# Kernel optimization log

Measured on AMD Instinct MI355X. Metric: run time of the kernel, lower is better.

Reference implementation:

```python
import jax, jax.numpy as jnp
import numpy as np

S, B, C = 1024, 2, 20
COORD, NOOBJ, NPRED = 5.0, 0.5, 5


def setup_inputs() -> dict:
    key = jax.random.key(0)
    k1, k2, k3 = jax.random.split(key, 3)
    pred = jax.random.normal(k1, (S, S, B * NPRED + C), dtype=jnp.float32)
    # target: box part uniform in [0,1) (w,h must be >=0 for sqrt), classes one-hot
    box_t = jax.random.uniform(k2, (S, S, B * NPRED), dtype=jnp.float32)
    cls_idx = jax.random.randint(k3, (S, S), 0, C)
    cls_t = jax.nn.one_hot(cls_idx, C, dtype=jnp.float32)
    target = jnp.concatenate([box_t, cls_t], axis=-1)
    return {"pred": pred, "target": target}


def reference(pred, target):
    # boxes: [S, S, B, 5] with (conf, x, y, w, h)
    boxes_p = pred[..., : B * NPRED].reshape(S, S, B, NPRED)
    boxes_t = target[..., : B * NPRED].reshape(S, S, B, NPRED)

    conf_p, x_p, y_p = boxes_p[..., 0], boxes_p[..., 1], boxes_p[..., 2]
    w_p = jnp.sqrt(jnp.abs(boxes_p[..., 3]))
    h_p = jnp.sqrt(jnp.abs(boxes_p[..., 4]))

    conf_t, x_t, y_t = boxes_t[..., 0], boxes_t[..., 1], boxes_t[..., 2]
    w_t = jnp.sqrt(boxes_t[..., 3])
    h_t = jnp.sqrt(boxes_t[..., 4])

    xy_loss = jnp.sum((jnp.square(x_t - x_p) + jnp.square(y_t - y_p)) * conf_t)
    box_loss = jnp.sum((jnp.square(w_t - w_p) + jnp.square(h_t - h_p)) * conf_t)
    conf_sq = jnp.square(conf_t - conf_p)
    confidence_loss = jnp.sum(conf_sq * conf_t)
    noobj_confidence_loss = jnp.sum(conf_sq * (1.0 - conf_t))

    # class loss: only cells whose target class vector sums to exactly 1.0
    pred_cls = pred[..., B * NPRED :].reshape(S * S, C)
    tgt_cls = target[..., B * NPRED :].reshape(S * S, C)
    cell_mask = (jnp.sum(tgt_cls, axis=-1) == 1.0).astype(pred.dtype)  # [S*S]
    per_cell = jnp.sum(jnp.square(tgt_cls) - jnp.square(pred_cls), axis=-1)
    cls_loss = jnp.sum(per_cell * cell_mask)

    return COORD * xy_loss + COORD * box_loss + confidence_loss + noobj_confidence_loss + cls_loss
```

## Files before the change

kernel.cpp:

```cpp
#include <hip/hip_runtime.h>


constexpr int CH         = 30;
constexpr int NCELL      = 1024 * 1024;
constexpr int BLOCK      = 256;
constexpr int TILE_CELLS = 128;
constexpr int TPF        = TILE_CELLS * CH;
constexpr int GRID       = 512;
constexpr int NTILES     = NCELL / TILE_CELLS;
constexpr int NIT        = NTILES / GRID;

__device__ __forceinline__ float wave_reduce_sum(float v) {
#pragma unroll
    for (int off = 32; off > 0; off >>= 1)
        v += __shfl_down(v, off, 64);
    return v;
}

__global__ __launch_bounds__(BLOCK, 2) void yolo_partial_kernel(
        const float* __restrict__ pred,
        const float* __restrict__ tgt,
        float* __restrict__ partial) {
    __shared__ float4 sbuf4[2][2 * TPF / 4];

    const int tid  = threadIdx.x;
    const int wv   = tid >> 6;
    const int ln   = tid & 63;
    const int cell = tid >> 1;
    const int half = tid & 1;

    float4 p0, p1, p2, t0, t1, t2;
    float2 p3, t3;
    float  p4, t4;

#define LOAD_TILE(tile)                                                      \
    do {                                                                     \
        const size_t tb = (size_t)(tile) * TPF;                              \
        const float4* pf4 = reinterpret_cast<const float4*>(pred + tb);      \
        const float4* tf4 = reinterpret_cast<const float4*>(tgt  + tb);      \
        const float2* pf2 = reinterpret_cast<const float2*>(pred + tb);      \
        const float2* tf2 = reinterpret_cast<const float2*>(tgt  + tb);      \
        p0 = pf4[0 * 256 + tid];  t0 = tf4[0 * 256 + tid];                   \
        p1 = pf4[1 * 256 + tid];  t1 = tf4[1 * 256 + tid];                   \
        p2 = pf4[2 * 256 + tid];  t2 = tf4[2 * 256 + tid];                   \
        p3 = pf2[1536 + tid];     t3 = tf2[1536 + tid];                      \
        p4 = pred[tb + 3584 + tid]; t4 = tgt[tb + 3584 + tid];               \
    } while (0)

#define STORE_TILE(b)                                                        \
    do {                                                                     \
        float*  sf  = reinterpret_cast<float*>(&sbuf4[(b)][0]);              \
        float4* sp4 = reinterpret_cast<float4*>(sf);                         \
        float4* st4 = reinterpret_cast<float4*>(sf + TPF);                   \
        float2* sp2 = reinterpret_cast<float2*>(sf);                         \
        float2* st2 = reinterpret_cast<float2*>(sf + TPF);                   \
        sp4[0 * 256 + tid] = p0;  st4[0 * 256 + tid] = t0;                   \
        sp4[1 * 256 + tid] = p1;  st4[1 * 256 + tid] = t1;                   \
        sp4[2 * 256 + tid] = p2;  st4[2 * 256 + tid] = t2;                   \
        sp2[1536 + tid] = p3;     st2[1536 + tid] = t3;                      \
        sf[3584 + tid] = p4;      sf[TPF + 3584 + tid] = t4;                 \
    } while (0)

    int t = blockIdx.x;
    LOAD_TILE(t);
    STORE_TILE(0);
    __syncthreads();

    float acc = 0.0f;
    for (int it = 0; it < NIT; ++it) {
        const int cur = it & 1;
        const bool havenext = (it + 1 < NIT);

        if (havenext) LOAD_TILE(t + GRID);
        __builtin_amdgcn_sched_barrier(0);

        const float* bf = reinterpret_cast<const float*>(&sbuf4[cur][0]);
        const float* pp = bf + cell * CH;
        const float* tt = bf + TPF + cell * CH;

        {
            const int o = 5 * half;
            const float conf_p = pp[o + 0];
            const float x_p    = pp[o + 1];
            const float y_p    = pp[o + 2];
            const float w_p    = sqrtf(fabsf(pp[o + 3]));
            const float h_p    = sqrtf(fabsf(pp[o + 4]));
            const float conf_t = tt[o + 0];
            const float x_t    = tt[o + 1];
            const float y_t    = tt[o + 2];
            const float w_t    = sqrtf(tt[o + 3]);
            const float h_t    = sqrtf(tt[o + 4]);

            const float dx = x_t - x_p, dy = y_t - y_p;
            const float dw = w_t - w_p, dh = h_t - h_p;
            const float dc = conf_t - conf_p;

            acc += 5.0f * ((dx * dx + dy * dy) * conf_t)
                 + 5.0f * ((dw * dw + dh * dh) * conf_t)
                 + dc * dc;
        }

        {
            float ssum = 0.0f, per_cell = 0.0f;
            const int co = 10 + 10 * half;
#pragma unroll
            for (int k = 0; k < 10; ++k) {
                const float tc = tt[co + k];
                const float pc = pp[co + k];
                ssum     += tc;
                per_cell += tc * tc - pc * pc;
            }
            const float tot = ssum + __shfl_xor(ssum, 1, 64);
            acc += (tot == 1.0f) ? per_cell : 0.0f;
        }

        if (havenext) STORE_TILE(cur ^ 1);
        __syncthreads();
        t += GRID;
    }

    __shared__ float red[BLOCK / 64];
    float v = wave_reduce_sum(acc);
    if (ln == 0) red[wv] = v;
    __syncthreads();
    if (wv == 0) {
        v = (ln < (BLOCK / 64)) ? red[ln] : 0.0f;
        v = wave_reduce_sum(v);
        if (ln == 0) partial[blockIdx.x] = v;
    }
#undef LOAD_TILE
#undef STORE_TILE
}

__global__ __launch_bounds__(256) void yolo_final_kernel(
        const float* __restrict__ partial,
        float* __restrict__ out,
        int n) {
    float acc = 0.0f;
    for (int i = threadIdx.x; i < n; i += 256)
        acc += partial[i];

    __shared__ float red[4];
    const int lane = threadIdx.x & 63;
    const int wid  = threadIdx.x >> 6;
    float v = wave_reduce_sum(acc);
    if (lane == 0) red[wid] = v;
    __syncthreads();
    if (wid == 0) {
        v = (lane < 4) ? red[lane] : 0.0f;
        v = wave_reduce_sum(v);
        if (lane == 0) out[0] = v;
    }
}

extern "C" void kernel_launch(void* const* d_in, const int* in_sizes, int n_in,
                              void* d_out, int out_size, void* d_ws, size_t ws_size,
                              hipStream_t stream) {
    const float* pred = (const float*)d_in[0];
    const float* tgt  = (const float*)d_in[1];
    float* out        = (float*)d_out;
    float* partial    = (float*)d_ws;

    yolo_partial_kernel<<<GRID, BLOCK, 0, stream>>>(pred, tgt, partial);
    yolo_final_kernel<<<1, 256, 0, stream>>>(partial, out, GRID);
}
```

Before: 43.43 us.

## Use triple-buffered LDS pipeline with smaller tiles and more blocks

Halves the tile to 64 cells so 256 threads cover four lanes per cell. Pred and target now share one flat load plan. It moves to a three-stage LDS ring buffer, so each tile is stored a full iteration after its load is issued, letting global loads overlap two compute phases. It also raises the grid to 768 blocks with three blocks per CU. The intent is more memory-level parallelism and more latency hiding, at the cost of more LDS per block, an uneven tile split across blocks, and an extra shuffle for the class-sum reduction.

```diff
diff --git a/kernel.cpp b/kernel.cpp
--- a/kernel.cpp
+++ b/kernel.cpp
@@ -4,11 +4,11 @@
 constexpr int CH         = 30;
 constexpr int NCELL      = 1024 * 1024;
 constexpr int BLOCK      = 256;
-constexpr int TILE_CELLS = 128;
+constexpr int TILE_CELLS = 64;
 constexpr int TPF        = TILE_CELLS * CH;
-constexpr int GRID       = 512;
+constexpr int BUFFLOATS  = 2 * TPF;
 constexpr int NTILES     = NCELL / TILE_CELLS;
-constexpr int NIT        = NTILES / GRID;
+constexpr int GRID       = 768;
 
 __device__ __forceinline__ float wave_reduce_sum(float v) {
 #pragma unroll
@@ -17,69 +17,68 @@
     return v;
 }
 
-__global__ __launch_bounds__(BLOCK, 2) void yolo_partial_kernel(
+__global__ __launch_bounds__(BLOCK, 3) void yolo_partial_kernel(
         const float* __restrict__ pred,
         const float* __restrict__ tgt,
         float* __restrict__ partial) {
-    __shared__ float4 sbuf4[2][2 * TPF / 4];
+    __shared__ float4 sbuf4[3 * BUFFLOATS / 4];
 
     const int tid  = threadIdx.x;
     const int wv   = tid >> 6;
     const int ln   = tid & 63;
-    const int cell = tid >> 1;
-    const int half = tid & 1;
+    const int cell = tid >> 2;
+    const int q    = tid & 3;
 
-    float4 p0, p1, p2, t0, t1, t2;
-    float2 p3, t3;
-    float  p4, t4;
+    float4 c0, c1, c2;
+    float2 c3;
+    float  c4;
 
-#define LOAD_TILE(tile)                                                      \
-    do {                                                                     \
-        const size_t tb = (size_t)(tile) * TPF;                              \
-        const float4* pf4 = reinterpret_cast<const float4*>(pred + tb);      \
-        const float4* tf4 = reinterpret_cast<const float4*>(tgt  + tb);      \
-        const float2* pf2 = reinterpret_cast<const float2*>(pred + tb);      \
-        const float2* tf2 = reinterpret_cast<const float2*>(tgt  + tb);      \
-        p0 = pf4[0 * 256 + tid];  t0 = tf4[0 * 256 + tid];                   \
-        p1 = pf4[1 * 256 + tid];  t1 = tf4[1 * 256 + tid];                   \
-        p2 = pf4[2 * 256 + tid];  t2 = tf4[2 * 256 + tid];                   \
-        p3 = pf2[1536 + tid];     t3 = tf2[1536 + tid];                      \
-        p4 = pred[tb + 3584 + tid]; t4 = tgt[tb + 3584 + tid];               \
+#define LOAD_TILE(tile)                                                       \
+    do {                                                                      \
+        const size_t tb = (size_t)(tile) * TPF;                               \
+        const float* pb = pred + tb;                                          \
+        const float* gb = tgt + tb;                                           \
+        c0 = *reinterpret_cast<const float4*>(pb + 4 * tid);                  \
+        const float* s1 = (tid < 224) ? (pb + 1024 + 4 * tid)                 \
+                                      : (gb + (4 * tid - 896));               \
+        c1 = *reinterpret_cast<const float4*>(s1);                            \
+        c2 = *reinterpret_cast<const float4*>(gb + 128 + 4 * tid);            \
+        c3 = *reinterpret_cast<const float2*>(gb + 1152 + 2 * tid);           \
+        c4 = gb[1664 + tid];                                                  \
     } while (0)
 
-#define STORE_TILE(b)                                                        \
-    do {                                                                     \
-        float*  sf  = reinterpret_cast<float*>(&sbuf4[(b)][0]);              \
-        float4* sp4 = reinterpret_cast<float4*>(sf);                         \
-        float4* st4 = reinterpret_cast<float4*>(sf + TPF);                   \
-        float2* sp2 = reinterpret_cast<float2*>(sf);                         \
-        float2* st2 = reinterpret_cast<float2*>(sf + TPF);                   \
-        sp4[0 * 256 + tid] = p0;  st4[0 * 256 + tid] = t0;                   \
-        sp4[1 * 256 + tid] = p1;  st4[1 * 256 + tid] = t1;                   \
-        sp4[2 * 256 + tid] = p2;  st4[2 * 256 + tid] = t2;                   \
-        sp2[1536 + tid] = p3;     st2[1536 + tid] = t3;                      \
-        sf[3584 + tid] = p4;      sf[TPF + 3584 + tid] = t4;                 \
+#define STORE_TILE(b)                                                         \
+    do {                                                                      \
+        float* sf = reinterpret_cast<float*>(&sbuf4[0]) + (b) * BUFFLOATS;    \
+        float4* s4 = reinterpret_cast<float4*>(sf);                           \
+        s4[0 * 256 + tid] = c0;                                               \
+        s4[1 * 256 + tid] = c1;                                               \
+        s4[2 * 256 + tid] = c2;                                               \
+        reinterpret_cast<float2*>(sf)[1536 + tid] = c3;                       \
+        sf[3584 + tid] = c4;                                                  \
     } while (0)
 
-    int t = blockIdx.x;
+    int t  = blockIdx.x;
+    int it = 0;
+
     LOAD_TILE(t);
     STORE_TILE(0);
+    if (t + GRID < NTILES) LOAD_TILE(t + GRID);
     __syncthreads();
 
     float acc = 0.0f;
-    for (int it = 0; it < NIT; ++it) {
-        const int cur = it & 1;
-        const bool havenext = (it + 1 < NIT);
-
-        if (havenext) LOAD_TILE(t + GRID);
+    for (;;) {
+        const int b_cur = it % 3;
+        if (t + GRID < NTILES)     STORE_TILE((it + 1) % 3);
+        if (t + 2 * GRID < NTILES) LOAD_TILE(t + 2 * GRID);
         __builtin_amdgcn_sched_barrier(0);
 
-        const float* bf = reinterpret_cast<const float*>(&sbuf4[cur][0]);
+        const float* bf = reinterpret_cast<const float*>(&sbuf4[0]) + b_cur * BUFFLOATS;
         const float* pp = bf + cell * CH;
         const float* tt = bf + TPF + cell * CH;
 
-        {
-            const int o = 5 * half;
+        if (q < 2) {
+            const int o = 5 * q;
             const float conf_p = pp[o + 0];
             const float x_p    = pp[o + 1];
             const float y_p    = pp[o + 2];
@@ -102,21 +101,24 @@
 
         {
             float ssum = 0.0f, per_cell = 0.0f;
-            const int co = 10 + 10 * half;
+            const int co = 10 + 5 * q;
 #pragma unroll
-            for (int k = 0; k < 10; ++k) {
+            for (int k = 0; k < 5; ++k) {
                 const float tc = tt[co + k];
                 const float pc = pp[co + k];
                 ssum     += tc;
                 per_cell += tc * tc - pc * pc;
             }
-            const float tot = ssum + __shfl_xor(ssum, 1, 64);
+            float tot = ssum;
+            tot += __shfl_xor(tot, 1, 64);
+            tot += __shfl_xor(tot, 2, 64);
             acc += (tot == 1.0f) ? per_cell : 0.0f;
         }
 
-        if (havenext) STORE_TILE(cur ^ 1);
         __syncthreads();
         t += GRID;
+        ++it;
+        if (t >= NTILES) break;
     }
 
     __shared__ float red[BLOCK / 64];
```

Result: no change. 44.26 us (+1.9%).
